# Kernel optimization log

Measured on AMD Instinct MI355X. Metric: run time of the kernel, lower is better.

The kernel has to match this reference:

```python
import jax, jax.numpy as jnp
import numpy as np

N = 12288
IN_DIM = 256
HID = 64
E = 393216


def _gcn_edges(edge_index, n):
    # add self-loops, compute symmetric normalization (PyG GCNConv default)
    src = jnp.concatenate([edge_index[0], jnp.arange(n, dtype=edge_index.dtype)])
    dst = jnp.concatenate([edge_index[1], jnp.arange(n, dtype=edge_index.dtype)])
    deg = jax.ops.segment_sum(jnp.ones_like(src, dtype=jnp.float32), dst, num_segments=n)
    dinv = jnp.where(deg > 0, jax.lax.rsqrt(deg), 0.0)
    norm = dinv[src] * dinv[dst]  # [E+N]
    return src, dst, norm


def _conv(h, src, dst, norm, W, b, n):
    # GCNConv: linear transform then normalized sparse aggregation
    h = h @ W
    agg = jax.ops.segment_sum(h[src] * norm[:, None], dst, num_segments=n)
    return agg + b


def setup_inputs() -> dict:
    key = jax.random.key(0)
    ks = jax.random.split(key, 16)
    x = jax.random.normal(ks[0], (N, IN_DIM), dtype=jnp.float32)
    edge_index = jax.random.randint(ks[1], (2, E), 0, N, dtype=jnp.int32)
    s = 0.05
    p = {
        'enc_W1': jax.random.normal(ks[2], (IN_DIM, HID), jnp.float32) * s,
        'enc_b1': jnp.zeros((HID,), jnp.float32),
        'enc_W2': jax.random.normal(ks[3], (HID, HID), jnp.float32) * s,
        'enc_b2': jnp.zeros((HID,), jnp.float32),
        'd1_W1': jax.random.normal(ks[4], (HID // 2, HID), jnp.float32) * s,
        'd1_b1': jnp.zeros((HID,), jnp.float32),
        'd1_W2': jax.random.normal(ks[5], (HID, IN_DIM), jnp.float32) * s,
        'd1_b2': jnp.zeros((IN_DIM,), jnp.float32),
        'd2_W1': jax.random.normal(ks[6], (HID // 2, HID), jnp.float32) * s,
        'd2_b1': jnp.zeros((HID,), jnp.float32),
        'd2_W2': jax.random.normal(ks[7], (HID, IN_DIM), jnp.float32) * s,
        'd2_b2': jnp.zeros((IN_DIM,), jnp.float32),
        's_W': jax.random.normal(ks[8], (HID // 2, HID), jnp.float32) * s,
        's_b': jnp.zeros((HID,), jnp.float32),
    }
    return dict(x=x, edge_index=edge_index, **p)


def reference(x, edge_index, enc_W1, enc_b1, enc_W2, enc_b2,
              d1_W1, d1_b1, d1_W2, d1_b2, d2_W1, d2_b1, d2_W2, d2_b2,
              s_W, s_b):
    n = x.shape[0]
    src, dst, norm = _gcn_edges(edge_index, n)

    def encoder(h):
        h = jax.nn.relu(_conv(h, src, dst, norm, enc_W1, enc_b1, n))
        return _conv(h, src, dst, norm, enc_W2, enc_b2, n)

    def dec1(h):
        h = jax.nn.relu(_conv(h, src, dst, norm, d1_W1, d1_b1, n))
        return _conv(h, src, dst, norm, d1_W2, d1_b2, n)

    def dec2(h):
        h = jax.nn.relu(_conv(h, src, dst, norm, d2_W1, d2_b1, n))
        return _conv(h, src, dst, norm, d2_W2, d2_b2, n)

    z = encoder(x)
    # counterfactual: flip sensitive attribute (column 0)
    x_cf = x.at[:, 0].set(1.0 - x[:, 0])
    z_cf = encoder(x_cf)

    h = z.shape[1] // 2
    z_s, z_ns = z[:, :h], z[:, h:]
    z_s_cf = z_cf[:, :h]

    x_s_hat = dec1(z_s)
    x_ns_hat = dec2(z_ns)
    x_s_cf_hat = dec1(z_s_cf)

    # DotProductDecoder: 1-layer GCN then dense inner-product decode (sigmoid_s=False)
    hs = _conv(z_ns, src, dst, norm, s_W, s_b, n)
    s_ = hs @ hs.T  # [N, N]

    return (z_s, z_ns, x_s_hat, x_ns_hat, x_s_cf_hat, s_)
```

## Files before the change

kernel.cpp:

```cpp
#include <hip/hip_runtime.h>

#define N_NODES 12288
#define IN_DIM_ 256
#define HID_ 64
#define E_EDGES 393216
#define TOT_EDGES (E_EDGES + N_NODES)

typedef __attribute__((ext_vector_type(8))) short bf16x8;
typedef __attribute__((ext_vector_type(16))) float f32x16;

__device__ inline unsigned short f2bf_rne(float f) {
  unsigned int u = __float_as_uint(f);
  unsigned int r = u + 0x7fffu + ((u >> 16) & 1u);
  return (unsigned short)(r >> 16);
}
__device__ inline float bf2f(unsigned short h) {
  return __uint_as_float(((unsigned int)h) << 16);
}


__global__ __launch_bounds__(256) void k_init(const float* __restrict__ x,
                                              int* __restrict__ deg,
                                              float* __restrict__ coef) {
  int i = blockIdx.x * 256 + threadIdx.x;
  if (i < N_NODES) {
    deg[i] = 1;
    coef[i] = 1.0f - 2.0f * x[(size_t)i * IN_DIM_];
  }
}

__global__ __launch_bounds__(256) void k_count(const int* __restrict__ dst,
                                               int* __restrict__ deg) {
  int e = blockIdx.x * 256 + threadIdx.x;
  if (e < E_EDGES) atomicAdd(&deg[dst[e]], 1);
}

__global__ __launch_bounds__(1024) void k_scan(const int* __restrict__ deg,
                                               int* __restrict__ rowptr,
                                               int* __restrict__ cursor,
                                               float* __restrict__ dinv) {
  __shared__ int sh[1024];
  const int t = threadIdx.x;
  int loc[12];
  int s = 0;
#pragma unroll
  for (int i = 0; i < 12; i++) {
    int d = deg[t * 12 + i];
    dinv[t * 12 + i] = 1.0f / sqrtf((float)d);
    loc[i] = s;
    s += d;
  }
  sh[t] = s;
  __syncthreads();
  for (int off = 1; off < 1024; off <<= 1) {
    int v = (t >= off) ? sh[t - off] : 0;
    __syncthreads();
    sh[t] += v;
    __syncthreads();
  }
  int base = sh[t] - s;
#pragma unroll
  for (int i = 0; i < 12; i++) {
    int v = base + loc[i];
    rowptr[t * 12 + i] = v;
    cursor[t * 12 + i] = v;
  }
  if (t == 1023) rowptr[N_NODES] = sh[1023];
}

__global__ __launch_bounds__(256) void k_fill(const int* __restrict__ src,
                                              const int* __restrict__ dst,
                                              const float* __restrict__ dinv,
                                              int* __restrict__ cursor,
                                              int* __restrict__ col,
                                              float* __restrict__ wgt) {
  int e = blockIdx.x * 256 + threadIdx.x;
  if (e < E_EDGES) {
    int s = src[e], d = dst[e];
    int pos = atomicAdd(&cursor[d], 1);
    col[pos] = s;
    wgt[pos] = dinv[s] * dinv[d];
  } else if (e < TOT_EDGES) {
    int i = e - E_EDGES;
    int pos = atomicAdd(&cursor[i], 1);
    col[pos] = i;
    float di = dinv[i];
    wgt[pos] = di * di;
  }
}


__global__ __launch_bounds__(256) void k_agg64_enc(
    const float* __restrict__ in, const int* __restrict__ rowptr,
    const int* __restrict__ col, const float* __restrict__ wgt,
    const float* __restrict__ bias, const float* __restrict__ coef,
    const float* __restrict__ wrow, float* __restrict__ out0,
    float* __restrict__ out1) {
  const int lane = threadIdx.x & 63;
  int node = blockIdx.x * 4 + (threadIdx.x >> 6);
  node = __builtin_amdgcn_readfirstlane(node);
  const int slice = blockIdx.y;
  const float wr = slice ? wrow[lane] : 0.0f;
  const int start = rowptr[node];
  const int end = rowptr[node + 1];
  float a0 = 0.0f, a1 = 0.0f, a2 = 0.0f, a3 = 0.0f;
  int e = start;
  for (; e + 8 <= end; e += 8) {
    int c0 = col[e + 0], c1 = col[e + 1], c2 = col[e + 2], c3 = col[e + 3];
    int c4 = col[e + 4], c5 = col[e + 5], c6 = col[e + 6], c7 = col[e + 7];
    float w0 = wgt[e + 0], w1 = wgt[e + 1], w2 = wgt[e + 2], w3 = wgt[e + 3];
    float w4 = wgt[e + 4], w5 = wgt[e + 5], w6 = wgt[e + 6], w7 = wgt[e + 7];
    float v0 = in[(size_t)c0 * 64 + lane];
    float v1 = in[(size_t)c1 * 64 + lane];
    float v2 = in[(size_t)c2 * 64 + lane];
    float v3 = in[(size_t)c3 * 64 + lane];
    float v4 = in[(size_t)c4 * 64 + lane];
    float v5 = in[(size_t)c5 * 64 + lane];
    float v6 = in[(size_t)c6 * 64 + lane];
    float v7 = in[(size_t)c7 * 64 + lane];
    v0 = fmaf(coef[c0], wr, v0);
    v1 = fmaf(coef[c1], wr, v1);
    v2 = fmaf(coef[c2], wr, v2);
    v3 = fmaf(coef[c3], wr, v3);
    v4 = fmaf(coef[c4], wr, v4);
    v5 = fmaf(coef[c5], wr, v5);
    v6 = fmaf(coef[c6], wr, v6);
    v7 = fmaf(coef[c7], wr, v7);
    a0 = fmaf(w0, v0, a0);
    a1 = fmaf(w1, v1, a1);
    a2 = fmaf(w2, v2, a2);
    a3 = fmaf(w3, v3, a3);
    a0 = fmaf(w4, v4, a0);
    a1 = fmaf(w5, v5, a1);
    a2 = fmaf(w6, v6, a2);
    a3 = fmaf(w7, v7, a3);
  }
  for (; e < end; ++e) {
    int c = col[e];
    float v = in[(size_t)c * 64 + lane];
    v = fmaf(coef[c], wr, v);
    a0 = fmaf(wgt[e], v, a0);
  }
  float acc = (a0 + a1) + (a2 + a3) + bias[lane];
  acc = fmaxf(acc, 0.0f);
  (slice ? out1 : out0)[(size_t)node * 64 + lane] = acc;
}

__global__ __launch_bounds__(256) void k_agg_z(
    const float* __restrict__ in64, const float* __restrict__ in32,
    const int* __restrict__ rowptr, const int* __restrict__ col,
    const float* __restrict__ wgt, const float* __restrict__ bias,
    float* __restrict__ out_zs, float* __restrict__ out_zns,
    float* __restrict__ out_zscf) {
  if (blockIdx.y == 0) {
    const int lane = threadIdx.x & 63;
    int node = blockIdx.x * 4 + (threadIdx.x >> 6);
    node = __builtin_amdgcn_readfirstlane(node);
    const int start = rowptr[node];
    const int end = rowptr[node + 1];
    float a0 = 0.0f, a1 = 0.0f, a2 = 0.0f, a3 = 0.0f;
    int e = start;
    for (; e + 8 <= end; e += 8) {
      int c0 = col[e + 0], c1 = col[e + 1], c2 = col[e + 2], c3 = col[e + 3];
      int c4 = col[e + 4], c5 = col[e + 5], c6 = col[e + 6], c7 = col[e + 7];
      float w0 = wgt[e + 0], w1 = wgt[e + 1], w2 = wgt[e + 2], w3 = wgt[e + 3];
      float w4 = wgt[e + 4], w5 = wgt[e + 5], w6 = wgt[e + 6], w7 = wgt[e + 7];
      float v0 = in64[(size_t)c0 * 64 + lane];
      float v1 = in64[(size_t)c1 * 64 + lane];
      float v2 = in64[(size_t)c2 * 64 + lane];
      float v3 = in64[(size_t)c3 * 64 + lane];
      float v4 = in64[(size_t)c4 * 64 + lane];
      float v5 = in64[(size_t)c5 * 64 + lane];
      float v6 = in64[(size_t)c6 * 64 + lane];
      float v7 = in64[(size_t)c7 * 64 + lane];
      a0 = fmaf(w0, v0, a0);
      a1 = fmaf(w1, v1, a1);
      a2 = fmaf(w2, v2, a2);
      a3 = fmaf(w3, v3, a3);
      a0 = fmaf(w4, v4, a0);
      a1 = fmaf(w5, v5, a1);
      a2 = fmaf(w6, v6, a2);
      a3 = fmaf(w7, v7, a3);
    }
    for (; e < end; ++e) {
      int c = col[e];
      a0 = fmaf(wgt[e], in64[(size_t)c * 64 + lane], a0);
    }
    float acc = (a0 + a1) + (a2 + a3) + bias[lane];
    if (lane < 32)
      out_zs[(size_t)node * 32 + lane] = acc;
    else
      out_zns[(size_t)node * 32 + (lane - 32)] = acc;
  } else {
    if (blockIdx.x >= 1536) return;
    const int lane = threadIdx.x & 31;
    const int node = blockIdx.x * 8 + (threadIdx.x >> 5);
    const int start = rowptr[node];
    const int end = rowptr[node + 1];
    float a0 = 0.0f, a1 = 0.0f, a2 = 0.0f, a3 = 0.0f;
    int e = start;
    for (; e + 8 <= end; e += 8) {
      int c0 = col[e + 0], c1 = col[e + 1], c2 = col[e + 2], c3 = col[e + 3];
      int c4 = col[e + 4], c5 = col[e + 5], c6 = col[e + 6], c7 = col[e + 7];
      float w0 = wgt[e + 0], w1 = wgt[e + 1], w2 = wgt[e + 2], w3 = wgt[e + 3];
      float w4 = wgt[e + 4], w5 = wgt[e + 5], w6 = wgt[e + 6], w7 = wgt[e + 7];
      a0 = fmaf(w0, in32[(size_t)c0 * 32 + lane], a0);
      a1 = fmaf(w1, in32[(size_t)c1 * 32 + lane], a1);
      a2 = fmaf(w2, in32[(size_t)c2 * 32 + lane], a2);
      a3 = fmaf(w3, in32[(size_t)c3 * 32 + lane], a3);
      a0 = fmaf(w4, in32[(size_t)c4 * 32 + lane], a0);
      a1 = fmaf(w5, in32[(size_t)c5 * 32 + lane], a1);
      a2 = fmaf(w6, in32[(size_t)c6 * 32 + lane], a2);
      a3 = fmaf(w7, in32[(size_t)c7 * 32 + lane], a3);
    }
    for (; e < end; ++e)
      a0 = fmaf(wgt[e], in32[(size_t)col[e] * 32 + lane], a0);
    out_zscf[(size_t)node * 32 + lane] = (a0 + a1) + (a2 + a3) + bias[lane];
  }
}

__global__ __launch_bounds__(256) void k_agg64_dec3(
    const float* __restrict__ in0, const float* __restrict__ in1,
    const float* __restrict__ in2, const int* __restrict__ rowptr,
    const int* __restrict__ col, const float* __restrict__ wgt,
    float* __restrict__ out0, float* __restrict__ out1,
    float* __restrict__ out2) {
  const int lane = threadIdx.x & 63;
  int node = blockIdx.x * 4 + (threadIdx.x >> 6);
  node = __builtin_amdgcn_readfirstlane(node);
  const int slice = blockIdx.y;
  const float* __restrict__ in = slice == 0 ? in0 : (slice == 1 ? in1 : in2);
  float* __restrict__ out = slice == 0 ? out0 : (slice == 1 ? out1 : out2);
  const int start = rowptr[node];
  const int end = rowptr[node + 1];
  float a0 = 0.0f, a1 = 0.0f, a2 = 0.0f, a3 = 0.0f;
  int e = start;
  for (; e + 8 <= end; e += 8) {
    int c0 = col[e + 0], c1 = col[e + 1], c2 = col[e + 2], c3 = col[e + 3];
    int c4 = col[e + 4], c5 = col[e + 5], c6 = col[e + 6], c7 = col[e + 7];
    float w0 = wgt[e + 0], w1 = wgt[e + 1], w2 = wgt[e + 2], w3 = wgt[e + 3];
    float w4 = wgt[e + 4], w5 = wgt[e + 5], w6 = wgt[e + 6], w7 = wgt[e + 7];
    float v0 = in[(size_t)c0 * 64 + lane];
    float v1 = in[(size_t)c1 * 64 + lane];
    float v2 = in[(size_t)c2 * 64 + lane];
    float v3 = in[(size_t)c3 * 64 + lane];
    float v4 = in[(size_t)c4 * 64 + lane];
    float v5 = in[(size_t)c5 * 64 + lane];
    float v6 = in[(size_t)c6 * 64 + lane];
    float v7 = in[(size_t)c7 * 64 + lane];
    a0 = fmaf(w0, v0, a0);
    a1 = fmaf(w1, v1, a1);
    a2 = fmaf(w2, v2, a2);
    a3 = fmaf(w3, v3, a3);
    a0 = fmaf(w4, v4, a0);
    a1 = fmaf(w5, v5, a1);
    a2 = fmaf(w6, v6, a2);
    a3 = fmaf(w7, v7, a3);
  }
  for (; e < end; ++e) {
    int c = col[e];
    a0 = fmaf(wgt[e], in[(size_t)c * 64 + lane], a0);
  }
  float acc = (a0 + a1) + (a2 + a3);
  out[(size_t)node * 64 + lane] = acc;
}

__global__ __launch_bounds__(256) void k_agg32_b3(
    const float* __restrict__ in0, const float* __restrict__ in1,
    const float* __restrict__ in2, const int* __restrict__ rowptr,
    const int* __restrict__ col, const float* __restrict__ wgt,
    float* __restrict__ out0, float* __restrict__ out1,
    float* __restrict__ out2) {
  const int lane = threadIdx.x & 31;
  const int node = blockIdx.x * 8 + (threadIdx.x >> 5);
  const int slice = blockIdx.y;
  const float* __restrict__ in = slice == 0 ? in0 : (slice == 1 ? in1 : in2);
  float* __restrict__ out = slice == 0 ? out0 : (slice == 1 ? out1 : out2);
  const int start = rowptr[node];
  const int end = rowptr[node + 1];
  float a0 = 0.0f, a1 = 0.0f, a2 = 0.0f, a3 = 0.0f;
  int e = start;
  for (; e + 8 <= end; e += 8) {
    int c0 = col[e + 0], c1 = col[e + 1], c2 = col[e + 2], c3 = col[e + 3];
    int c4 = col[e + 4], c5 = col[e + 5], c6 = col[e + 6], c7 = col[e + 7];
    float w0 = wgt[e + 0], w1 = wgt[e + 1], w2 = wgt[e + 2], w3 = wgt[e + 3];
    float w4 = wgt[e + 4], w5 = wgt[e + 5], w6 = wgt[e + 6], w7 = wgt[e + 7];
    a0 = fmaf(w0, in[(size_t)c0 * 32 + lane], a0);
    a1 = fmaf(w1, in[(size_t)c1 * 32 + lane], a1);
    a2 = fmaf(w2, in[(size_t)c2 * 32 + lane], a2);
    a3 = fmaf(w3, in[(size_t)c3 * 32 + lane], a3);
    a0 = fmaf(w4, in[(size_t)c4 * 32 + lane], a0);
    a1 = fmaf(w5, in[(size_t)c5 * 32 + lane], a1);
    a2 = fmaf(w6, in[(size_t)c6 * 32 + lane], a2);
    a3 = fmaf(w7, in[(size_t)c7 * 32 + lane], a3);
  }
  for (; e < end; ++e) a0 = fmaf(wgt[e], in[(size_t)col[e] * 32 + lane], a0);
  out[(size_t)node * 32 + lane] = (a0 + a1) + (a2 + a3);
}


template <int K, int KC, int NF, int LDW, int RPT, bool BIAS, bool RELU>
__global__ __launch_bounds__(256) void k_gemm_v4(const float* __restrict__ A,
                                                 const float* __restrict__ W,
                                                 const float* __restrict__ bias,
                                                 float* __restrict__ C) {
  __shared__ float Ws[KC * NF];
  constexpr int G = 256 / NF;
  const int c = threadIdx.x % NF;
  const int rg = threadIdx.x / NF;
  const int r0 = blockIdx.x * (G * RPT) + rg * RPT;
  float acc[RPT];
#pragma unroll
  for (int i = 0; i < RPT; i++) acc[i] = 0.0f;
  for (int k0 = 0; k0 < K; k0 += KC) {
    for (int t = threadIdx.x; t < KC * NF; t += 256)
      Ws[t] = W[(k0 + t / NF) * LDW + (t % NF)];
    __syncthreads();
#pragma unroll 2
    for (int k = 0; k < KC; k += 4) {
      float4 a[RPT];
#pragma unroll
      for (int i = 0; i < RPT; i++)
        a[i] = *(const float4*)&A[(size_t)(r0 + i) * K + k0 + k];
      float w0 = Ws[(k + 0) * NF + c];
      float w1 = Ws[(k + 1) * NF + c];
      float w2 = Ws[(k + 2) * NF + c];
      float w3 = Ws[(k + 3) * NF + c];
#pragma unroll
      for (int i = 0; i < RPT; i++) {
        acc[i] = fmaf(a[i].x, w0, acc[i]);
        acc[i] = fmaf(a[i].y, w1, acc[i]);
        acc[i] = fmaf(a[i].z, w2, acc[i]);
        acc[i] = fmaf(a[i].w, w3, acc[i]);
      }
    }
    __syncthreads();
  }
  float b = BIAS ? bias[c] : 0.0f;
#pragma unroll
  for (int i = 0; i < RPT; i++) {
    float v = acc[i] + b;
    if (RELU) v = fmaxf(v, 0.0f);
    C[(size_t)(r0 + i) * NF + c] = v;
  }
}

__global__ __launch_bounds__(256) void k_gemm_enc2(
    const float* __restrict__ A0, const float* __restrict__ A1,
    const float* __restrict__ W, float* __restrict__ C0,
    float* __restrict__ C1) {
  __shared__ float Ws[64 * 64];
  const int slice = blockIdx.y;
  const float* __restrict__ A = slice ? A1 : A0;
  for (int i = threadIdx.x; i < 64 * 64; i += 256) Ws[i] = W[i];
  __syncthreads();
  const int c = threadIdx.x & 63;
  const int rg = threadIdx.x >> 6;
  const int r0 = blockIdx.x * 16 + rg * 4;
  float acc[4];
#pragma unroll
  for (int i = 0; i < 4; i++) acc[i] = 0.0f;
#pragma unroll 2
  for (int k = 0; k < 64; k += 4) {
    float4 a[4];
#pragma unroll
    for (int i = 0; i < 4; i++)
      a[i] = *(const float4*)&A[(size_t)(r0 + i) * 64 + k];
    float w0 = Ws[(k + 0) * 64 + c];
    float w1 = Ws[(k + 1) * 64 + c];
    float w2 = Ws[(k + 2) * 64 + c];
    float w3 = Ws[(k + 3) * 64 + c];
#pragma unroll
    for (int i = 0; i < 4; i++) {
      acc[i] = fmaf(a[i].x, w0, acc[i]);
      acc[i] = fmaf(a[i].y, w1, acc[i]);
      acc[i] = fmaf(a[i].z, w2, acc[i]);
      acc[i] = fmaf(a[i].w, w3, acc[i]);
    }
  }
  if (slice == 0) {
#pragma unroll
    for (int i = 0; i < 4; i++) C0[(size_t)(r0 + i) * 64 + c] = acc[i];
  } else if (c < 32) {
#pragma unroll
    for (int i = 0; i < 4; i++) C1[(size_t)(r0 + i) * 32 + c] = acc[i];
  }
}

__global__ __launch_bounds__(256) void k_gemm_u4(
    const float* __restrict__ A0, const float* __restrict__ A1,
    const float* __restrict__ A2, const float* __restrict__ W0,
    const float* __restrict__ W1, const float* __restrict__ W2,
    const float* __restrict__ W3, const float* __restrict__ b0,
    const float* __restrict__ b1, const float* __restrict__ b2,
    const float* __restrict__ b3, float* __restrict__ C0,
    float* __restrict__ C1, float* __restrict__ C2,
    unsigned short* __restrict__ hi, unsigned short* __restrict__ lo) {
  __shared__ float Ws[32 * 64];
  const int slice = blockIdx.y;
  const float* __restrict__ A =
      slice == 0 ? A0 : (slice == 1 ? A1 : A2);
  const float* __restrict__ W =
      slice == 0 ? W0 : (slice == 1 ? W1 : (slice == 2 ? W2 : W3));
  const float* __restrict__ bias =
      slice == 0 ? b0 : (slice == 1 ? b1 : (slice == 2 ? b2 : b3));
  for (int i = threadIdx.x; i < 32 * 64; i += 256) Ws[i] = W[i];
  __syncthreads();
  const int c = threadIdx.x & 63;
  const int rg = threadIdx.x >> 6;
  const int r0 = blockIdx.x * 16 + rg * 4;
  float acc[4];
#pragma unroll
  for (int i = 0; i < 4; i++) acc[i] = 0.0f;
#pragma unroll 2
  for (int k = 0; k < 32; k += 4) {
    float4 a[4];
#pragma unroll
    for (int i = 0; i < 4; i++)
      a[i] = *(const float4*)&A[(size_t)(r0 + i) * 32 + k];
    float w0 = Ws[(k + 0) * 64 + c];
    float w1 = Ws[(k + 1) * 64 + c];
    float w2 = Ws[(k + 2) * 64 + c];
    float w3 = Ws[(k + 3) * 64 + c];
#pragma unroll
    for (int i = 0; i < 4; i++) {
      acc[i] = fmaf(a[i].x, w0, acc[i]);
      acc[i] = fmaf(a[i].y, w1, acc[i]);
      acc[i] = fmaf(a[i].z, w2, acc[i]);
      acc[i] = fmaf(a[i].w, w3, acc[i]);
    }
  }
  float b = bias[c];
  if (slice < 3) {
    float* __restrict__ C = slice == 0 ? C0 : (slice == 1 ? C1 : C2);
#pragma unroll
    for (int i = 0; i < 4; i++)
      C[(size_t)(r0 + i) * 64 + c] = fmaxf(acc[i] + b, 0.0f);
  } else {
#pragma unroll
    for (int i = 0; i < 4; i++) {
      float v = acc[i] + b;
      unsigned short h = f2bf_rne(v);
      float l = v - bf2f(h);
      hi[(size_t)(r0 + i) * 64 + c] = h;
      lo[(size_t)(r0 + i) * 64 + c] = f2bf_rne(l);
    }
  }
}

__global__ __launch_bounds__(256) void k_gemm_o3(
    const float* __restrict__ A0, const float* __restrict__ A1,
    const float* __restrict__ A2, const float* __restrict__ W0,
    const float* __restrict__ W1, const float* __restrict__ W2,
    const float* __restrict__ b0, const float* __restrict__ b1,
    const float* __restrict__ b2, float* __restrict__ C0,
    float* __restrict__ C1, float* __restrict__ C2) {
  __shared__ float Ws[16 * 256];
  const int slice = blockIdx.y;
  const float* __restrict__ A = slice == 0 ? A0 : (slice == 1 ? A1 : A2);
  const float* __restrict__ W = slice == 0 ? W0 : (slice == 1 ? W1 : W2);
  const float* __restrict__ bias = slice == 0 ? b0 : (slice == 1 ? b1 : b2);
  float* __restrict__ C = slice == 0 ? C0 : (slice == 1 ? C1 : C2);
  const int c = threadIdx.x & 63;
  const int rg = threadIdx.x >> 6;
  const int r0 = blockIdx.x * 16 + rg * 4;
  float acc[4][4];
#pragma unroll
  for (int i = 0; i < 4; i++)
#pragma unroll
    for (int j = 0; j < 4; j++) acc[i][j] = 0.0f;
  for (int k0 = 0; k0 < 64; k0 += 16) {
    for (int t = threadIdx.x; t < 16 * 256; t += 256)
      Ws[t] = W[(k0 + (t >> 8)) * 256 + (t & 255)];
    __syncthreads();
#pragma unroll
    for (int k = 0; k < 16; k += 4) {
      float4 a[4];
#pragma unroll
      for (int i = 0; i < 4; i++)
        a[i] = *(const float4*)&A[(size_t)(r0 + i) * 64 + k0 + k];
#pragma unroll
      for (int kk = 0; kk < 4; kk++) {
        float w0 = Ws[(k + kk) * 256 + c];
        float w1 = Ws[(k + kk) * 256 + c + 64];
        float w2 = Ws[(k + kk) * 256 + c + 128];
        float w3 = Ws[(k + kk) * 256 + c + 192];
#pragma unroll
        for (int i = 0; i < 4; i++) {
          float av = kk == 0 ? a[i].x : (kk == 1 ? a[i].y : (kk == 2 ? a[i].z : a[i].w));
          acc[i][0] = fmaf(av, w0, acc[i][0]);
          acc[i][1] = fmaf(av, w1, acc[i][1]);
          acc[i][2] = fmaf(av, w2, acc[i][2]);
          acc[i][3] = fmaf(av, w3, acc[i][3]);
        }
      }
    }
    __syncthreads();
  }
  float bb0 = bias[c], bb1 = bias[c + 64], bb2 = bias[c + 128], bb3 = bias[c + 192];
#pragma unroll
  for (int i = 0; i < 4; i++) {
    size_t base = (size_t)(r0 + i) * 256;
    C[base + c] = acc[i][0] + bb0;
    C[base + c + 64] = acc[i][1] + bb1;
    C[base + c + 128] = acc[i][2] + bb2;
    C[base + c + 192] = acc[i][3] + bb3;
  }
}


__global__ __launch_bounds__(256) void k_syrk_mfma(
    const unsigned short* __restrict__ hhi, const unsigned short* __restrict__ hlo,
    float* __restrict__ out) {
  const int tid = threadIdx.x;
  const int lane = tid & 63;
  const int wave = tid >> 6;
  const int wy = wave >> 1, wx = wave & 1;
  const int m = lane & 31;
  const int koff = (lane >> 5) * 8;
  const size_t rb = (size_t)blockIdx.y * 128 + wy * 64;
  const size_t cb = (size_t)blockIdx.x * 128 + wx * 64;
  f32x16 acc[2][2];
#pragma unroll
  for (int i = 0; i < 2; i++)
#pragma unroll
    for (int j = 0; j < 2; j++) acc[i][j] = (f32x16)(0.0f);
#pragma unroll
  for (int k0 = 0; k0 < 64; k0 += 16) {
    bf16x8 ah[2], al[2], bh[2], bl[2];
#pragma unroll
    for (int t = 0; t < 2; t++) {
      size_t ra = (rb + t * 32 + m) * 64 + k0 + koff;
      ah[t] = *(const bf16x8*)(hhi + ra);
      al[t] = *(const bf16x8*)(hlo + ra);
      size_t rc = (cb + t * 32 + m) * 64 + k0 + koff;
      bh[t] = *(const bf16x8*)(hhi + rc);
      bl[t] = *(const bf16x8*)(hlo + rc);
    }
#pragma unroll
    for (int i = 0; i < 2; i++)
#pragma unroll
      for (int j = 0; j < 2; j++) {
        acc[i][j] = __builtin_amdgcn_mfma_f32_32x32x16_bf16(ah[i], bh[j], acc[i][j], 0, 0, 0);
        acc[i][j] = __builtin_amdgcn_mfma_f32_32x32x16_bf16(ah[i], bl[j], acc[i][j], 0, 0, 0);
        acc[i][j] = __builtin_amdgcn_mfma_f32_32x32x16_bf16(al[i], bh[j], acc[i][j], 0, 0, 0);
      }
  }
  const int rowoff = 4 * (lane >> 5);
  const int colc = lane & 31;
#pragma unroll
  for (int i = 0; i < 2; i++)
#pragma unroll
    for (int j = 0; j < 2; j++)
#pragma unroll
      for (int r = 0; r < 16; r++) {
        size_t row = rb + i * 32 + (r & 3) + 8 * (r >> 2) + rowoff;
        out[row * 12288 + cb + j * 32 + colc] = acc[i][j][r];
      }
}


extern "C" void kernel_launch(void* const* d_in, const int* in_sizes, int n_in,
                              void* d_out, int out_size, void* d_ws,
                              size_t ws_size, hipStream_t stream) {
  (void)in_sizes; (void)n_in; (void)out_size; (void)ws_size;
  const float* x = (const float*)d_in[0];
  const int* ei = (const int*)d_in[1];
  const int* src = ei;
  const int* dst = ei + E_EDGES;
  const float* eW1 = (const float*)d_in[2];
  const float* eb1 = (const float*)d_in[3];
  const float* eW2 = (const float*)d_in[4];
  const float* eb2 = (const float*)d_in[5];
  const float* d1W1 = (const float*)d_in[6];
  const float* d1b1 = (const float*)d_in[7];
  const float* d1W2 = (const float*)d_in[8];
  const float* d1b2 = (const float*)d_in[9];
  const float* d2W1 = (const float*)d_in[10];
  const float* d2b1 = (const float*)d_in[11];
  const float* d2W2 = (const float*)d_in[12];
  const float* d2b2 = (const float*)d_in[13];
  const float* sW = (const float*)d_in[14];
  const float* sb = (const float*)d_in[15];

  float* out = (float*)d_out;
  float* out_zs = out;
  float* out_zns = out + 393216;
  float* out_xs = out + 786432;
  float* out_xns = out + 3932160;
  float* out_xscf = out + 7077888;
  float* out_s = out + 10223616;

  char* w = (char*)d_ws;
  size_t o = 0;
  auto alloc = [&](size_t bytes) -> void* {
    void* p = (void*)(w + o);
    o += (bytes + 255) & ~(size_t)255;
    return p;
  };
  int* deg = (int*)alloc(N_NODES * 4);
  int* rowptr = (int*)alloc((N_NODES + 1) * 4);
  int* cursor = (int*)alloc(N_NODES * 4);
  int* col = (int*)alloc(TOT_EDGES * 4);
  float* wgt = (float*)alloc(TOT_EDGES * 4);
  float* dinv = (float*)alloc(N_NODES * 4);
  float* coef = (float*)alloc(N_NODES * 4);
  const size_t B64 = (size_t)N_NODES * 64 * 4;
  const size_t B32 = (size_t)N_NODES * 32 * 4;
  float* slotA = (float*)alloc(B64);
  float* slotB = (float*)alloc(B64);
  float* slotC = (float*)alloc(B64);
  float* slotU3 = (float*)alloc(B64);
  float* slotG2 = (float*)alloc(B64);
  float* slotG3 = (float*)alloc(B64);
  float* t32 = (float*)alloc(B32);
  float* zscf = (float*)alloc(B32);
  float* gs = (float*)alloc(B32);
  float* gscf = (float*)alloc(B32);
  float* gns = (float*)alloc(B32);
  unsigned short* hhi = (unsigned short*)alloc((size_t)N_NODES * 64 * 2);
  unsigned short* hlo = (unsigned short*)alloc((size_t)N_NODES * 64 * 2);

  k_init<<<48, 256, 0, stream>>>(x, deg, coef);
  k_count<<<1536, 256, 0, stream>>>(dst, deg);
  k_scan<<<1, 1024, 0, stream>>>(deg, rowptr, cursor, dinv);
  k_fill<<<1584, 256, 0, stream>>>(src, dst, dinv, cursor, col, wgt);

  k_gemm_v4<256, 64, 64, 64, 4, false, false><<<768, 256, 0, stream>>>(
      x, eW1, nullptr, slotA);
  k_agg64_enc<<<dim3(3072, 2), 256, 0, stream>>>(slotA, rowptr, col, wgt, eb1,
                                                 coef, eW1, slotB, slotC);
  k_gemm_enc2<<<dim3(768, 2), 256, 0, stream>>>(slotB, slotC, eW2, slotA, t32);
  k_agg_z<<<dim3(3072, 2), 256, 0, stream>>>(slotA, t32, rowptr, col, wgt,
                                             eb2, out_zs, out_zns, zscf);

  k_agg32_b3<<<dim3(1536, 3), 256, 0, stream>>>(out_zs, zscf, out_zns, rowptr,
                                                col, wgt, gs, gscf, gns);
  k_gemm_u4<<<dim3(768, 4), 256, 0, stream>>>(gs, gscf, gns, d1W1, d1W1, d2W1,
                                              sW, d1b1, d1b1, d2b1, sb, slotB,
                                              slotC, slotU3, hhi, hlo);
  k_agg64_dec3<<<dim3(3072, 3), 256, 0, stream>>>(slotB, slotC, slotU3, rowptr,
                                                  col, wgt, slotA, slotG2,
                                                  slotG3);
  k_gemm_o3<<<dim3(768, 3), 256, 0, stream>>>(slotA, slotG2, slotG3, d1W2,
                                              d1W2, d2W2, d1b2, d1b2, d2b2,
                                              out_xs, out_xscf, out_xns);

  k_syrk_mfma<<<dim3(96, 96), 256, 0, stream>>>(hhi, hlo, out_s);
}
```

Before: 988.0 us.

## Fuse sparse aggregation with following dense transforms in encoder and decoders

Each aggregation kernel now runs the next small dense matmul itself, using the aggregated row held in shared memory. This removes the separate GEMM launches and their intermediate buffer round-trips. The encoder also computes the counterfactual branch in the same pass by accumulating the weighted coef sum as a scalar instead of re-aggregating. The trade-off is per-block weight loading into shared memory and a row-at-a-time matvec with less reuse than a tiled GEMM.

```diff
diff --git a/kernel.cpp b/kernel.cpp
--- a/kernel.cpp
+++ b/kernel.cpp
@@ -90,20 +90,66 @@
 }
 
 
-__global__ __launch_bounds__(256) void k_agg64_enc(
+template <int K, int KC, int NF, int LDW, int RPT>
+__global__ __launch_bounds__(256) void k_gemm_v4(const float* __restrict__ A,
+                                                 const float* __restrict__ W,
+                                                 float* __restrict__ C) {
+  __shared__ float Ws[KC * NF];
+  constexpr int G = 256 / NF;
+  const int c = threadIdx.x % NF;
+  const int rg = threadIdx.x / NF;
+  const int r0 = blockIdx.x * (G * RPT) + rg * RPT;
+  float acc[RPT];
+#pragma unroll
+  for (int i = 0; i < RPT; i++) acc[i] = 0.0f;
+  for (int k0 = 0; k0 < K; k0 += KC) {
+    __syncthreads();
+    for (int t = threadIdx.x; t < KC * NF; t += 256)
+      Ws[t] = W[(k0 + t / NF) * LDW + (t % NF)];
+    __syncthreads();
+#pragma unroll 2
+    for (int k = 0; k < KC; k += 4) {
+      float4 a[RPT];
+#pragma unroll
+      for (int i = 0; i < RPT; i++)
+        a[i] = *(const float4*)&A[(size_t)(r0 + i) * K + k0 + k];
+      float w0 = Ws[(k + 0) * NF + c];
+      float w1 = Ws[(k + 1) * NF + c];
+      float w2 = Ws[(k + 2) * NF + c];
+      float w3 = Ws[(k + 3) * NF + c];
+#pragma unroll
+      for (int i = 0; i < RPT; i++) {
+        acc[i] = fmaf(a[i].x, w0, acc[i]);
+        acc[i] = fmaf(a[i].y, w1, acc[i]);
+        acc[i] = fmaf(a[i].z, w2, acc[i]);
+        acc[i] = fmaf(a[i].w, w3, acc[i]);
+      }
+    }
+  }
+#pragma unroll
+  for (int i = 0; i < RPT; i++) C[(size_t)(r0 + i) * NF + c] = acc[i];
+}
+
+
+__global__ __launch_bounds__(256) void k_enc_fused(
     const float* __restrict__ in, const int* __restrict__ rowptr,
     const int* __restrict__ col, const float* __restrict__ wgt,
-    const float* __restrict__ bias, const float* __restrict__ coef,
-    const float* __restrict__ wrow, float* __restrict__ out0,
-    float* __restrict__ out1) {
+    const float* __restrict__ b1, const float* __restrict__ coef,
+    const float* __restrict__ wrow, const float* __restrict__ eW2,
+    float* __restrict__ HWe2, float* __restrict__ t32) {
+  __shared__ float Ws[64 * 64];
+  __shared__ float h1s[4][64];
+  __shared__ float h1cfs[4][64];
+  for (int i = threadIdx.x; i < 64 * 64; i += 256) Ws[i] = eW2[i];
+
   const int lane = threadIdx.x & 63;
-  int node = blockIdx.x * 4 + (threadIdx.x >> 6);
-  node = __builtin_amdgcn_readfirstlane(node);
-  const int slice = blockIdx.y;
-  const float wr = slice ? wrow[lane] : 0.0f;
+  const int wv = threadIdx.x >> 6;
+  int node = __builtin_amdgcn_readfirstlane(blockIdx.x * 4 + wv);
   const int start = rowptr[node];
   const int end = rowptr[node + 1];
-  float a0 = 0.0f, a1 = 0.0f, a2 = 0.0f, a3 = 0.0f;
+  const float wr = wrow[lane];
+  float a0 = 0, a1 = 0, a2 = 0, a3 = 0;
+  float s0 = 0, s1 = 0, s2 = 0, s3 = 0;
   int e = start;
   for (; e + 8 <= end; e += 8) {
     int c0 = col[e + 0], c1 = col[e + 1], c2 = col[e + 2], c3 = col[e + 3];
@@ -118,14 +164,6 @@
     float v5 = in[(size_t)c5 * 64 + lane];
     float v6 = in[(size_t)c6 * 64 + lane];
     float v7 = in[(size_t)c7 * 64 + lane];
-    v0 = fmaf(coef[c0], wr, v0);
-    v1 = fmaf(coef[c1], wr, v1);
-    v2 = fmaf(coef[c2], wr, v2);
-    v3 = fmaf(coef[c3], wr, v3);
-    v4 = fmaf(coef[c4], wr, v4);
-    v5 = fmaf(coef[c5], wr, v5);
-    v6 = fmaf(coef[c6], wr, v6);
-    v7 = fmaf(coef[c7], wr, v7);
     a0 = fmaf(w0, v0, a0);
     a1 = fmaf(w1, v1, a1);
     a2 = fmaf(w2, v2, a2);
@@ -134,17 +172,40 @@
     a1 = fmaf(w5, v5, a1);
     a2 = fmaf(w6, v6, a2);
     a3 = fmaf(w7, v7, a3);
+    s0 = fmaf(w0, coef[c0], s0);
+    s1 = fmaf(w1, coef[c1], s1);
+    s2 = fmaf(w2, coef[c2], s2);
+    s3 = fmaf(w3, coef[c3], s3);
+    s0 = fmaf(w4, coef[c4], s0);
+    s1 = fmaf(w5, coef[c5], s1);
+    s2 = fmaf(w6, coef[c6], s2);
+    s3 = fmaf(w7, coef[c7], s3);
   }
   for (; e < end; ++e) {
     int c = col[e];
-    float v = in[(size_t)c * 64 + lane];
-    v = fmaf(coef[c], wr, v);
-    a0 = fmaf(wgt[e], v, a0);
-  }
-  float acc = (a0 + a1) + (a2 + a3) + bias[lane];
-  acc = fmaxf(acc, 0.0f);
-  (slice ? out1 : out0)[(size_t)node * 64 + lane] = acc;
-}
+    float we = wgt[e];
+    a0 = fmaf(we, in[(size_t)c * 64 + lane], a0);
+    s0 = fmaf(we, coef[c], s0);
+  }
+  float acc = (a0 + a1) + (a2 + a3);
+  float s = (s0 + s1) + (s2 + s3);
+  float bb = b1[lane];
+  h1s[wv][lane] = fmaxf(acc + bb, 0.0f);
+  h1cfs[wv][lane] = fmaxf(fmaf(wr, s, acc) + bb, 0.0f);
+  __syncthreads();
+
+  float A2 = 0, A3 = 0;
+#pragma unroll 4
+  for (int k = 0; k < 64; ++k) {
+    float wv_ = Ws[k * 64 + lane];
+    A2 = fmaf(h1s[wv][k], wv_, A2);
+    A3 = fmaf(h1cfs[wv][k], wv_, A3);
+  }
+  size_t n = (size_t)blockIdx.x * 4 + wv;
+  HWe2[n * 64 + lane] = A2;
+  if (lane < 32) t32[n * 32 + lane] = A3;
+}
+
 
 __global__ __launch_bounds__(256) void k_agg_z(
     const float* __restrict__ in64, const float* __restrict__ in32,
@@ -158,7 +219,7 @@
     node = __builtin_amdgcn_readfirstlane(node);
     const int start = rowptr[node];
     const int end = rowptr[node + 1];
-    float a0 = 0.0f, a1 = 0.0f, a2 = 0.0f, a3 = 0.0f;
+    float a0 = 0, a1 = 0, a2 = 0, a3 = 0;
     int e = start;
     for (; e + 8 <= end; e += 8) {
       int c0 = col[e + 0], c1 = col[e + 1], c2 = col[e + 2], c3 = col[e + 3];
@@ -197,7 +258,7 @@
     const int node = blockIdx.x * 8 + (threadIdx.x >> 5);
     const int start = rowptr[node];
     const int end = rowptr[node + 1];
-    float a0 = 0.0f, a1 = 0.0f, a2 = 0.0f, a3 = 0.0f;
+    float a0 = 0, a1 = 0, a2 = 0, a3 = 0;
     int e = start;
     for (; e + 8 <= end; e += 8) {
       int c0 = col[e + 0], c1 = col[e + 1], c2 = col[e + 2], c3 = col[e + 3];
@@ -219,21 +280,100 @@
   }
 }
 
-__global__ __launch_bounds__(256) void k_agg64_dec3(
+
+__global__ __launch_bounds__(256) void k_u_fused(
     const float* __restrict__ in0, const float* __restrict__ in1,
     const float* __restrict__ in2, const int* __restrict__ rowptr,
     const int* __restrict__ col, const float* __restrict__ wgt,
-    float* __restrict__ out0, float* __restrict__ out1,
-    float* __restrict__ out2) {
+    const float* __restrict__ W01, const float* __restrict__ W2,
+    const float* __restrict__ Wh, const float* __restrict__ b01,
+    const float* __restrict__ b2, const float* __restrict__ bh,
+    float* __restrict__ o0, float* __restrict__ o1, float* __restrict__ o2,
+    unsigned short* __restrict__ hhi, unsigned short* __restrict__ hlo) {
+  __shared__ float Ws[32 * 64];
+  __shared__ float Ws2[32 * 64];
+  __shared__ float gsh[4][32];
+  const int y = blockIdx.y;
+  const float* __restrict__ in = y == 0 ? in0 : (y == 1 ? in1 : in2);
+  const float* __restrict__ W = y == 2 ? W2 : W01;
+  const float* __restrict__ bias = y == 2 ? b2 : b01;
+  for (int i = threadIdx.x; i < 32 * 64; i += 256) Ws[i] = W[i];
+  if (y == 2)
+    for (int i = threadIdx.x; i < 32 * 64; i += 256) Ws2[i] = Wh[i];
+
   const int lane = threadIdx.x & 63;
-  int node = blockIdx.x * 4 + (threadIdx.x >> 6);
-  node = __builtin_amdgcn_readfirstlane(node);
-  const int slice = blockIdx.y;
-  const float* __restrict__ in = slice == 0 ? in0 : (slice == 1 ? in1 : in2);
-  float* __restrict__ out = slice == 0 ? out0 : (slice == 1 ? out1 : out2);
+  const int wv = threadIdx.x >> 6;
+  const int feat = lane & 31;
+  const int half = lane >> 5;
+  int node = __builtin_amdgcn_readfirstlane(blockIdx.x * 4 + wv);
   const int start = rowptr[node];
   const int end = rowptr[node + 1];
-  float a0 = 0.0f, a1 = 0.0f, a2 = 0.0f, a3 = 0.0f;
+  float a0 = 0, a1 = 0, a2 = 0, a3 = 0;
+  int e = start;
+  for (; e + 8 <= end; e += 8) {
+    int c0 = col[e + 0 + half], c1 = col[e + 2 + half];
+    int c2 = col[e + 4 + half], c3 = col[e + 6 + half];
+    float w0 = wgt[e + 0 + half], w1 = wgt[e + 2 + half];
+    float w2 = wgt[e + 4 + half], w3 = wgt[e + 6 + half];
+    a0 = fmaf(w0, in[(size_t)c0 * 32 + feat], a0);
+    a1 = fmaf(w1, in[(size_t)c1 * 32 + feat], a1);
+    a2 = fmaf(w2, in[(size_t)c2 * 32 + feat], a2);
+    a3 = fmaf(w3, in[(size_t)c3 * 32 + feat], a3);
+  }
+  for (; e + 2 <= end; e += 2) {
+    int c = col[e + half];
+    a0 = fmaf(wgt[e + half], in[(size_t)c * 32 + feat], a0);
+  }
+  if (e < end && half == 0) {
+    int c = col[e];
+    a0 = fmaf(wgt[e], in[(size_t)c * 32 + feat], a0);
+  }
+  float tot = (a0 + a1) + (a2 + a3);
+  tot += __shfl_xor(tot, 32);
+  if (half == 0) gsh[wv][feat] = tot;
+  __syncthreads();
+
+  float A = 0, B = 0;
+#pragma unroll 4
+  for (int k = 0; k < 32; ++k) {
+    float g = gsh[wv][k];
+    A = fmaf(g, Ws[k * 64 + lane], A);
+    if (y == 2) B = fmaf(g, Ws2[k * 64 + lane], B);
+  }
+  size_t n = (size_t)blockIdx.x * 4 + wv;
+  float* __restrict__ o = y == 0 ? o0 : (y == 1 ? o1 : o2);
+  o[n * 64 + lane] = fmaxf(A + bias[lane], 0.0f);
+  if (y == 2) {
+    float v = B + bh[lane];
+    unsigned short h = f2bf_rne(v);
+    float l = v - bf2f(h);
+    hhi[n * 64 + lane] = h;
+    hlo[n * 64 + lane] = f2bf_rne(l);
+  }
+}
+
+
+__global__ __launch_bounds__(256) void k_dec_fused(
+    const float* __restrict__ in0, const float* __restrict__ in1,
+    const float* __restrict__ in2, const int* __restrict__ rowptr,
+    const int* __restrict__ col, const float* __restrict__ wgt,
+    const float* __restrict__ W01, const float* __restrict__ W2,
+    const float* __restrict__ b01, const float* __restrict__ b2,
+    float* __restrict__ o0, float* __restrict__ o1, float* __restrict__ o2) {
+  __shared__ float Wc[16 * 256];
+  __shared__ float gsh[4][64];
+  const int y = blockIdx.y;
+  const float* __restrict__ in = y == 0 ? in0 : (y == 1 ? in1 : in2);
+  const float* __restrict__ W = y == 2 ? W2 : W01;
+  const float* __restrict__ bias = y == 2 ? b2 : b01;
+  float* __restrict__ o = y == 0 ? o0 : (y == 1 ? o1 : o2);
+
+  const int lane = threadIdx.x & 63;
+  const int wv = threadIdx.x >> 6;
+  int node = __builtin_amdgcn_readfirstlane(blockIdx.x * 4 + wv);
+  const int start = rowptr[node];
+  const int end = rowptr[node + 1];
+  float a0 = 0, a1 = 0, a2 = 0, a3 = 0;
   int e = start;
   for (; e + 8 <= end; e += 8) {
     int c0 = col[e + 0], c1 = col[e + 1], c2 = col[e + 2], c3 = col[e + 3];
@@ -261,251 +401,28 @@
     int c = col[e];
     a0 = fmaf(wgt[e], in[(size_t)c * 64 + lane], a0);
   }
-  float acc = (a0 + a1) + (a2 + a3);
-  out[(size_t)node * 64 + lane] = acc;
-}
-
-__global__ __launch_bounds__(256) void k_agg32_b3(
-    const float* __restrict__ in0, const float* __restrict__ in1,
-    const float* __restrict__ in2, const int* __restrict__ rowptr,
-    const int* __restrict__ col, const float* __restrict__ wgt,
-    float* __restrict__ out0, float* __restrict__ out1,
-    float* __restrict__ out2) {
-  const int lane = threadIdx.x & 31;
-  const int node = blockIdx.x * 8 + (threadIdx.x >> 5);
-  const int slice = blockIdx.y;
-  const float* __restrict__ in = slice == 0 ? in0 : (slice == 1 ? in1 : in2);
-  float* __restrict__ out = slice == 0 ? out0 : (slice == 1 ? out1 : out2);
-  const int start = rowptr[node];
-  const int end = rowptr[node + 1];
-  float a0 = 0.0f, a1 = 0.0f, a2 = 0.0f, a3 = 0.0f;
-  int e = start;
-  for (; e + 8 <= end; e += 8) {
-    int c0 = col[e + 0], c1 = col[e + 1], c2 = col[e + 2], c3 = col[e + 3];
-    int c4 = col[e + 4], c5 = col[e + 5], c6 = col[e + 6], c7 = col[e + 7];
-    float w0 = wgt[e + 0], w1 = wgt[e + 1], w2 = wgt[e + 2], w3 = wgt[e + 3];
-    float w4 = wgt[e + 4], w5 = wgt[e + 5], w6 = wgt[e + 6], w7 = wgt[e + 7];
-    a0 = fmaf(w0, in[(size_t)c0 * 32 + lane], a0);
-    a1 = fmaf(w1, in[(size_t)c1 * 32 + lane], a1);
-    a2 = fmaf(w2, in[(size_t)c2 * 32 + lane], a2);
-    a3 = fmaf(w3, in[(size_t)c3 * 32 + lane], a3);
-    a0 = fmaf(w4, in[(size_t)c4 * 32 + lane], a0);
-    a1 = fmaf(w5, in[(size_t)c5 * 32 + lane], a1);
-    a2 = fmaf(w6, in[(size_t)c6 * 32 + lane], a2);
-    a3 = fmaf(w7, in[(size_t)c7 * 32 + lane], a3);
-  }
-  for (; e < end; ++e) a0 = fmaf(wgt[e], in[(size_t)col[e] * 32 + lane], a0);
-  out[(size_t)node * 32 + lane] = (a0 + a1) + (a2 + a3);
-}
-
-
-template <int K, int KC, int NF, int LDW, int RPT, bool BIAS, bool RELU>
-__global__ __launch_bounds__(256) void k_gemm_v4(const float* __restrict__ A,
-                                                 const float* __restrict__ W,
-                                                 const float* __restrict__ bias,
-                                                 float* __restrict__ C) {
-  __shared__ float Ws[KC * NF];
-  constexpr int G = 256 / NF;
-  const int c = threadIdx.x % NF;
-  const int rg = threadIdx.x / NF;
-  const int r0 = blockIdx.x * (G * RPT) + rg * RPT;
-  float acc[RPT];
-#pragma unroll
-  for (int i = 0; i < RPT; i++) acc[i] = 0.0f;
-  for (int k0 = 0; k0 < K; k0 += KC) {
-    for (int t = threadIdx.x; t < KC * NF; t += 256)
-      Ws[t] = W[(k0 + t / NF) * LDW + (t % NF)];
+  gsh[wv][lane] = (a0 + a1) + (a2 + a3);
+
+  float acc[4] = {0, 0, 0, 0};
+  for (int k0 = 0; k0 < 64; k0 += 16) {
     __syncthreads();
-#pragma unroll 2
-    for (int k = 0; k < KC; k += 4) {
-      float4 a[RPT];
-#pragma unroll
-      for (int i = 0; i < RPT; i++)
-        a[i] = *(const float4*)&A[(size_t)(r0 + i) * K + k0 + k];
-      float w0 = Ws[(k + 0) * NF + c];
-      float w1 = Ws[(k + 1) * NF + c];
-      float w2 = Ws[(k + 2) * NF + c];
-      float w3 = Ws[(k + 3) * NF + c];
-#pragma unroll
-      for (int i = 0; i < RPT; i++) {
-        acc[i] = fmaf(a[i].x, w0, acc[i]);
-        acc[i] = fmaf(a[i].y, w1, acc[i]);
-        acc[i] = fmaf(a[i].z, w2, acc[i]);
-        acc[i] = fmaf(a[i].w, w3, acc[i]);
-      }
+    for (int t = threadIdx.x; t < 16 * 256; t += 256)
+      Wc[t] = W[(k0 + (t >> 8)) * 256 + (t & 255)];
+    __syncthreads();
+#pragma unroll 4
+    for (int k = 0; k < 16; ++k) {
+      float g = gsh[wv][k0 + k];
+      acc[0] = fmaf(g, Wc[k * 256 + lane], acc[0]);
+      acc[1] = fmaf(g, Wc[k * 256 + lane + 64], acc[1]);
+      acc[2] = fmaf(g, Wc[k * 256 + lane + 128], acc[2]);
+      acc[3] = fmaf(g, Wc[k * 256 + lane + 192], acc[3]);
     }
-    __syncthreads();
-  }
-  float b = BIAS ? bias[c] : 0.0f;
-#pragma unroll
-  for (int i = 0; i < RPT; i++) {
-    float v = acc[i] + b;
-    if (RELU) v = fmaxf(v, 0.0f);
-    C[(size_t)(r0 + i) * NF + c] = v;
-  }
-}
-
-__global__ __launch_bounds__(256) void k_gemm_enc2(
-    const float* __restrict__ A0, const float* __restrict__ A1,
-    const float* __restrict__ W, float* __restrict__ C0,
-    float* __restrict__ C1) {
-  __shared__ float Ws[64 * 64];
-  const int slice = blockIdx.y;
-  const float* __restrict__ A = slice ? A1 : A0;
-  for (int i = threadIdx.x; i < 64 * 64; i += 256) Ws[i] = W[i];
-  __syncthreads();
-  const int c = threadIdx.x & 63;
-  const int rg = threadIdx.x >> 6;
-  const int r0 = blockIdx.x * 16 + rg * 4;
-  float acc[4];
-#pragma unroll
-  for (int i = 0; i < 4; i++) acc[i] = 0.0f;
-#pragma unroll 2
-  for (int k = 0; k < 64; k += 4) {
-    float4 a[4];
-#pragma unroll
-    for (int i = 0; i < 4; i++)
-      a[i] = *(const float4*)&A[(size_t)(r0 + i) * 64 + k];
-    float w0 = Ws[(k + 0) * 64 + c];
-    float w1 = Ws[(k + 1) * 64 + c];
-    float w2 = Ws[(k + 2) * 64 + c];
-    float w3 = Ws[(k + 3) * 64 + c];
-#pragma unroll
-    for (int i = 0; i < 4; i++) {
-      acc[i] = fmaf(a[i].x, w0, acc[i]);
-      acc[i] = fmaf(a[i].y, w1, acc[i]);
-      acc[i] = fmaf(a[i].z, w2, acc[i]);
-      acc[i] = fmaf(a[i].w, w3, acc[i]);
-    }
-  }
-  if (slice == 0) {
-#pragma unroll
-    for (int i = 0; i < 4; i++) C0[(size_t)(r0 + i) * 64 + c] = acc[i];
-  } else if (c < 32) {
-#pragma unroll
-    for (int i = 0; i < 4; i++) C1[(size_t)(r0 + i) * 32 + c] = acc[i];
-  }
-}
-
-__global__ __launch_bounds__(256) void k_gemm_u4(
-    const float* __restrict__ A0, const float* __restrict__ A1,
-    const float* __restrict__ A2, const float* __restrict__ W0,
-    const float* __restrict__ W1, const float* __restrict__ W2,
-    const float* __restrict__ W3, const float* __restrict__ b0,
-    const float* __restrict__ b1, const float* __restrict__ b2,
-    const float* __restrict__ b3, float* __restrict__ C0,
-    float* __restrict__ C1, float* __restrict__ C2,
-    unsigned short* __restrict__ hi, unsigned short* __restrict__ lo) {
-  __shared__ float Ws[32 * 64];
-  const int slice = blockIdx.y;
-  const float* __restrict__ A =
-      slice == 0 ? A0 : (slice == 1 ? A1 : A2);
-  const float* __restrict__ W =
-      slice == 0 ? W0 : (slice == 1 ? W1 : (slice == 2 ? W2 : W3));
-  const float* __restrict__ bias =
-      slice == 0 ? b0 : (slice == 1 ? b1 : (slice == 2 ? b2 : b3));
-  for (int i = threadIdx.x; i < 32 * 64; i += 256) Ws[i] = W[i];
-  __syncthreads();
-  const int c = threadIdx.x & 63;
-  const int rg = threadIdx.x >> 6;
-  const int r0 = blockIdx.x * 16 + rg * 4;
-  float acc[4];
-#pragma unroll
-  for (int i = 0; i < 4; i++) acc[i] = 0.0f;
-#pragma unroll 2
-  for (int k = 0; k < 32; k += 4) {
-    float4 a[4];
-#pragma unroll
-    for (int i = 0; i < 4; i++)
-      a[i] = *(const float4*)&A[(size_t)(r0 + i) * 32 + k];
-    float w0 = Ws[(k + 0) * 64 + c];
-    float w1 = Ws[(k + 1) * 64 + c];
-    float w2 = Ws[(k + 2) * 64 + c];
-    float w3 = Ws[(k + 3) * 64 + c];
-#pragma unroll
-    for (int i = 0; i < 4; i++) {
-      acc[i] = fmaf(a[i].x, w0, acc[i]);
-      acc[i] = fmaf(a[i].y, w1, acc[i]);
-      acc[i] = fmaf(a[i].z, w2, acc[i]);
-      acc[i] = fmaf(a[i].w, w3, acc[i]);
-    }
-  }
-  float b = bias[c];
-  if (slice < 3) {
-    float* __restrict__ C = slice == 0 ? C0 : (slice == 1 ? C1 : C2);
-#pragma unroll
-    for (int i = 0; i < 4; i++)
-      C[(size_t)(r0 + i) * 64 + c] = fmaxf(acc[i] + b, 0.0f);
-  } else {
-#pragma unroll
-    for (int i = 0; i < 4; i++) {
-      float v = acc[i] + b;
-      unsigned short h = f2bf_rne(v);
-      float l = v - bf2f(h);
-      hi[(size_t)(r0 + i) * 64 + c] = h;
-      lo[(size_t)(r0 + i) * 64 + c] = f2bf_rne(l);
-    }
-  }
-}
-
-__global__ __launch_bounds__(256) void k_gemm_o3(
-    const float* __restrict__ A0, const float* __restrict__ A1,
-    const float* __restrict__ A2, const float* __restrict__ W0,
-    const float* __restrict__ W1, const float* __restrict__ W2,
-    const float* __restrict__ b0, const float* __restrict__ b1,
-    const float* __restrict__ b2, float* __restrict__ C0,
-    float* __restrict__ C1, float* __restrict__ C2) {
-  __shared__ float Ws[16 * 256];
-  const int slice = blockIdx.y;
-  const float* __restrict__ A = slice == 0 ? A0 : (slice == 1 ? A1 : A2);
-  const float* __restrict__ W = slice == 0 ? W0 : (slice == 1 ? W1 : W2);
-  const float* __restrict__ bias = slice == 0 ? b0 : (slice == 1 ? b1 : b2);
-  float* __restrict__ C = slice == 0 ? C0 : (slice == 1 ? C1 : C2);
-  const int c = threadIdx.x & 63;
-  const int rg = threadIdx.x >> 6;
-  const int r0 = blockIdx.x * 16 + rg * 4;
-  float acc[4][4];
-#pragma unroll
-  for (int i = 0; i < 4; i++)
-#pragma unroll
-    for (int j = 0; j < 4; j++) acc[i][j] = 0.0f;
-  for (int k0 = 0; k0 < 64; k0 += 16) {
-    for (int t = threadIdx.x; t < 16 * 256; t += 256)
-      Ws[t] = W[(k0 + (t >> 8)) * 256 + (t & 255)];
-    __syncthreads();
-#pragma unroll
-    for (int k = 0; k < 16; k += 4) {
-      float4 a[4];
-#pragma unroll
-      for (int i = 0; i < 4; i++)
-        a[i] = *(const float4*)&A[(size_t)(r0 + i) * 64 + k0 + k];
-#pragma unroll
-      for (int kk = 0; kk < 4; kk++) {
-        float w0 = Ws[(k + kk) * 256 + c];
-        float w1 = Ws[(k + kk) * 256 + c + 64];
-        float w2 = Ws[(k + kk) * 256 + c + 128];
-        float w3 = Ws[(k + kk) * 256 + c + 192];
-#pragma unroll
-        for (int i = 0; i < 4; i++) {
-          float av = kk == 0 ? a[i].x : (kk == 1 ? a[i].y : (kk == 2 ? a[i].z : a[i].w));
-          acc[i][0] = fmaf(av, w0, acc[i][0]);
-          acc[i][1] = fmaf(av, w1, acc[i][1]);
-          acc[i][2] = fmaf(av, w2, acc[i][2]);
-          acc[i][3] = fmaf(av, w3, acc[i][3]);
-        }
-      }
-    }
-    __syncthreads();
-  }
-  float bb0 = bias[c], bb1 = bias[c + 64], bb2 = bias[c + 128], bb3 = bias[c + 192];
-#pragma unroll
-  for (int i = 0; i < 4; i++) {
-    size_t base = (size_t)(r0 + i) * 256;
-    C[base + c] = acc[i][0] + bb0;
-    C[base + c + 64] = acc[i][1] + bb1;
-    C[base + c + 128] = acc[i][2] + bb2;
-    C[base + c + 192] = acc[i][3] + bb3;
-  }
+  }
+  size_t base = ((size_t)blockIdx.x * 4 + wv) * 256;
+  o[base + lane] = acc[0] + bias[lane];
+  o[base + lane + 64] = acc[1] + bias[lane + 64];
+  o[base + lane + 128] = acc[2] + bias[lane + 128];
+  o[base + lane + 192] = acc[3] + bias[lane + 192];
 }
 
 
@@ -611,13 +528,8 @@
   float* slotB = (float*)alloc(B64);
   float* slotC = (float*)alloc(B64);
   float* slotU3 = (float*)alloc(B64);
-  float* slotG2 = (float*)alloc(B64);
-  float* slotG3 = (float*)alloc(B64);
   float* t32 = (float*)alloc(B32);
   float* zscf = (float*)alloc(B32);
-  float* gs = (float*)alloc(B32);
-  float* gscf = (float*)alloc(B32);
-  float* gns = (float*)alloc(B32);
   unsigned short* hhi = (unsigned short*)alloc((size_t)N_NODES * 64 * 2);
   unsigned short* hlo = (unsigned short*)alloc((size_t)N_NODES * 64 * 2);
 
@@ -626,25 +538,18 @@
   k_scan<<<1, 1024, 0, stream>>>(deg, rowptr, cursor, dinv);
   k_fill<<<1584, 256, 0, stream>>>(src, dst, dinv, cursor, col, wgt);
 
-  k_gemm_v4<256, 64, 64, 64, 4, false, false><<<768, 256, 0, stream>>>(
-      x, eW1, nullptr, slotA);
-  k_agg64_enc<<<dim3(3072, 2), 256, 0, stream>>>(slotA, rowptr, col, wgt, eb1,
-                                                 coef, eW1, slotB, slotC);
-  k_gemm_enc2<<<dim3(768, 2), 256, 0, stream>>>(slotB, slotC, eW2, slotA, t32);
-  k_agg_z<<<dim3(3072, 2), 256, 0, stream>>>(slotA, t32, rowptr, col, wgt,
+  k_gemm_v4<256, 64, 64, 64, 4><<<768, 256, 0, stream>>>(x, eW1, slotA);
+  k_enc_fused<<<3072, 256, 0, stream>>>(slotA, rowptr, col, wgt, eb1, coef,
+                                        eW1, eW2, slotB, t32);
+  k_agg_z<<<dim3(3072, 2), 256, 0, stream>>>(slotB, t32, rowptr, col, wgt,
                                              eb2, out_zs, out_zns, zscf);
 
-  k_agg32_b3<<<dim3(1536, 3), 256, 0, stream>>>(out_zs, zscf, out_zns, rowptr,
-                                                col, wgt, gs, gscf, gns);
-  k_gemm_u4<<<dim3(768, 4), 256, 0, stream>>>(gs, gscf, gns, d1W1, d1W1, d2W1,
-                                              sW, d1b1, d1b1, d2b1, sb, slotB,
-                                              slotC, slotU3, hhi, hlo);
-  k_agg64_dec3<<<dim3(3072, 3), 256, 0, stream>>>(slotB, slotC, slotU3, rowptr,
-                                                  col, wgt, slotA, slotG2,
-                                                  slotG3);
-  k_gemm_o3<<<dim3(768, 3), 256, 0, stream>>>(slotA, slotG2, slotG3, d1W2,
-                                              d1W2, d2W2, d1b2, d1b2, d2b2,
-                                              out_xs, out_xscf, out_xns);
+  k_u_fused<<<dim3(3072, 3), 256, 0, stream>>>(
+      out_zs, zscf, out_zns, rowptr, col, wgt, d1W1, d2W1, sW, d1b1, d2b1, sb,
+      slotA, slotC, slotU3, hhi, hlo);
+  k_dec_fused<<<dim3(3072, 3), 256, 0, stream>>>(
+      slotA, slotC, slotU3, rowptr, col, wgt, d1W2, d2W2, d1b2, d2b2, out_xs,
+      out_xscf, out_xns);
 
   k_syrk_mfma<<<dim3(96, 96), 256, 0, stream>>>(hhi, hlo, out_s);
 }
```

Result: faster. 965.9 us (-2.2%).
